# Kernel tuning notes

Hardware: AMD Instinct MI355X
Metric: run time of the kernel (lower is better)

The kernel has to match this reference:

```python
import jax, jax.numpy as jnp
import numpy as np

N, IN_DIM, HID, K, TOP_M = 131072, 512, 128, 256, 32


def setup_inputs() -> dict:
    key = jax.random.key(0)
    ks = jax.random.split(key, 16)
    s_in = 1.0 / np.sqrt(IN_DIM)
    s_h = 1.0 / np.sqrt(HID)
    return {
        "h0": jax.random.normal(ks[0], (N, IN_DIM), jnp.float32),
        "W1": jax.random.uniform(ks[1], (IN_DIM, HID), jnp.float32, -s_in, s_in),
        "b1": jax.random.uniform(ks[2], (HID,), jnp.float32, -s_in, s_in),
        "W2": jax.random.uniform(ks[3], (HID, HID), jnp.float32, -s_h, s_h),
        "b2": jax.random.uniform(ks[4], (HID,), jnp.float32, -s_h, s_h),
        "Wm": jax.random.uniform(ks[5], (HID, HID), jnp.float32, -s_h, s_h),
        "bm": jax.random.uniform(ks[6], (HID,), jnp.float32, -s_h, s_h),
        "Wt": jax.random.uniform(ks[7], (HID, HID), jnp.float32, -s_h, s_h),
        "bt": jax.random.uniform(ks[8], (HID,), jnp.float32, -s_h, s_h),
        "Wp": jax.random.uniform(ks[9], (HID, HID), jnp.float32, -s_h, s_h),
        "bp": jax.random.uniform(ks[10], (HID,), jnp.float32, -s_h, s_h),
        "cb_m": jax.random.normal(ks[11], (K, HID), jnp.float32),
        "cb_t": jax.random.normal(ks[12], (K, HID), jnp.float32),
        "cb_p": jax.random.normal(ks[13], (K, HID), jnp.float32),
        "ws": jax.random.uniform(ks[14], (HID,), jnp.float32, -s_h, s_h),
        "wb": jax.random.uniform(ks[15], (1,), jnp.float32, -s_h, s_h),
    }


def _l2n(x):
    return x / jnp.clip(jnp.linalg.norm(x, axis=-1, keepdims=True), 1e-12, None)


def _cos_dist(z, cb):
    # cosine-sim VQ codebook 'distance': [N, K] similarity matrix
    return jnp.einsum("nd,kd->nk", _l2n(z), _l2n(cb))


def reference(h0, W1, b1, W2, b2, Wm, bm, Wt, bt, Wp, bp, cb_m, cb_t, cb_p, ws, wb):
    # encoder MLP
    H = jax.nn.relu(jax.nn.relu(h0 @ W1 + b1) @ W2 + b2)  # [N, HID]
    dist_m = _cos_dist(H @ Wm + bm, cb_m)  # [N, K]
    dist_t = _cos_dist(H @ Wt + bt, cb_t)
    dist_p = _cos_dist(H @ Wp + bp, cb_p)
    # default path: argmin over codebook axis
    k_m = jnp.argmin(dist_m, axis=-1)
    k_t = jnp.argmin(dist_t, axis=-1)
    k_p = jnp.argmin(dist_p, axis=-1)
    codes = jnp.stack([k_m, k_t, k_p], axis=-1)  # [N, 3]
    alpha = jax.nn.sigmoid(H @ ws + wb[0])  # [N]
    n = codes.shape[0]
    M = min(TOP_M, n)
    _, key_idx = jax.lax.top_k(alpha, M)
    key_idx = jnp.clip(key_idx, 0, n - 1)
    return codes, key_idx, codes[key_idx]
```

## Files before the change

kernel.cpp:

```cpp
#include <hip/hip_runtime.h>

#define NROWS   131072
#define INDIM   512
#define HIDD    128
#define KCB     256

#define OFF_A     0u
#define OFF_CV    98304u
#define OFF_LOG   99072u
#define OFF_HIST  230144u
#define OFF_META  295680u
#define OFF_LISTA 295696u
#define OFF_LISTB 295824u
#define LISTB_CAP 2048u

__device__ __forceinline__ unsigned order_key(float f) {
    unsigned u = __float_as_uint(f);
    return u ^ ((u & 0x80000000u) ? 0xFFFFFFFFu : 0x80000000u);
}

__global__ __launch_bounds__(256) void vq_precompute(
    const float* __restrict__ Wm, const float* __restrict__ bm,
    const float* __restrict__ Wt, const float* __restrict__ bt,
    const float* __restrict__ Wp, const float* __restrict__ bp,
    const float* __restrict__ cbm, const float* __restrict__ cbt, const float* __restrict__ cbp,
    float* __restrict__ A, float* __restrict__ cv)
{
    const int c  = blockIdx.x >> 3;
    const int jg = (blockIdx.x & 7) * 16;
    const float* W  = (c == 0) ? Wm  : (c == 1) ? Wt  : Wp;
    const float* bb = (c == 0) ? bm  : (c == 1) ? bt  : bp;
    const float* cb = (c == 0) ? cbm : (c == 1) ? cbt : cbp;
    const int k = threadIdx.x;
    const float4* cbr = (const float4*)(cb + (size_t)k * HIDD);
    float s = 0.f;
    for (int d = 0; d < HIDD / 4; ++d) {
        float4 x = cbr[d];
        s += x.x * x.x + x.y * x.y + x.z * x.z + x.w * x.w;
    }
    const float rn = 1.f / fmaxf(sqrtf(s), 1e-12f);
    for (int j = jg; j < jg + 16; ++j) {
        const float4* wr = (const float4*)(W + (size_t)j * HIDD);
        float acc = 0.f;
        for (int d = 0; d < HIDD / 4; ++d) {
            float4 x = cbr[d]; float4 w = wr[d];
            acc += x.x * w.x + x.y * w.y + x.z * w.z + x.w * w.w;
        }
        A[((size_t)c * HIDD + j) * KCB + k] = acc * rn;
    }
    if (jg == 0) {
        const float4* br = (const float4*)bb;
        float acc = 0.f;
        for (int d = 0; d < HIDD / 4; ++d) {
            float4 x = cbr[d]; float4 w = br[d];
            acc += x.x * w.x + x.y * w.y + x.z * w.z + x.w * w.w;
        }
        cv[(size_t)c * KCB + k] = acc * rn;
    }
}

__global__ __launch_bounds__(256, 3) void vq_main(
    const float* __restrict__ h0, const float* __restrict__ W1, const float* __restrict__ b1,
    const float* __restrict__ W2, const float* __restrict__ b2,
    const float* __restrict__ A, const float* __restrict__ cv, const float* __restrict__ wsv,
    int* __restrict__ codes, float* __restrict__ logits, unsigned* __restrict__ hist)
{
    __shared__ float T[HIDD * 64];
    __shared__ float S[4096];

    const int t  = threadIdx.x;
    const int tx = t & 15;
    const int ty = t >> 4;
    const int row0 = blockIdx.x * 64;

    {
        float acc[4][8] = {};
        for (int kc = 0; kc < INDIM; kc += 16) {
            {
                const int rr = t >> 2, kq = (t & 3) * 4;
                float4 v = *(const float4*)(h0 + (size_t)(row0 + rr) * INDIM + kc + kq);
                S[(kq + 0) * 64 + rr] = v.x;
                S[(kq + 1) * 64 + rr] = v.y;
                S[(kq + 2) * 64 + rr] = v.z;
                S[(kq + 3) * 64 + rr] = v.w;
                const float4* src = (const float4*)(W1 + (size_t)kc * HIDD);
                float4* dst = (float4*)(S + 1024);
                dst[t]       = src[t];
                dst[t + 256] = src[t + 256];
            }
            __syncthreads();
            #pragma unroll 8
            for (int k = 0; k < 16; ++k) {
                float4 av  = *(const float4*)&S[k * 64 + 4 * ty];
                float4 b0  = *(const float4*)&S[1024 + k * HIDD + 4 * tx];
                float4 b1v = *(const float4*)&S[1024 + k * HIDD + 64 + 4 * tx];
                float aa[4] = {av.x, av.y, av.z, av.w};
                float bbv[8] = {b0.x, b0.y, b0.z, b0.w, b1v.x, b1v.y, b1v.z, b1v.w};
                #pragma unroll
                for (int r = 0; r < 4; ++r)
                    #pragma unroll
                    for (int j = 0; j < 8; ++j)
                        acc[r][j] = fmaf(aa[r], bbv[j], acc[r][j]);
            }
            __syncthreads();
        }
        float4 bv0 = *(const float4*)&b1[4 * tx];
        float4 bv1 = *(const float4*)&b1[4 * tx + 64];
        float ba[8] = {bv0.x, bv0.y, bv0.z, bv0.w, bv1.x, bv1.y, bv1.z, bv1.w};
        #pragma unroll
        for (int i = 0; i < 2; ++i)
            #pragma unroll
            for (int j = 0; j < 4; ++j) {
                const int c = 4 * tx + 64 * i + j;
                float4 col;
                col.x = fmaxf(acc[0][i * 4 + j] + ba[i * 4 + j], 0.f);
                col.y = fmaxf(acc[1][i * 4 + j] + ba[i * 4 + j], 0.f);
                col.z = fmaxf(acc[2][i * 4 + j] + ba[i * 4 + j], 0.f);
                col.w = fmaxf(acc[3][i * 4 + j] + ba[i * 4 + j], 0.f);
                *(float4*)&T[c * 64 + 4 * ty] = col;
            }
    }
    __syncthreads();

    {
        float acc[4][8] = {};
        for (int kc = 0; kc < HIDD; kc += 16) {
            const float4* src = (const float4*)(W2 + (size_t)kc * HIDD);
            float4* dst = (float4*)S;
            dst[t]       = src[t];
            dst[t + 256] = src[t + 256];
            __syncthreads();
            #pragma unroll 8
            for (int k = 0; k < 16; ++k) {
                float4 av  = *(const float4*)&T[(kc + k) * 64 + 4 * ty];
                float4 b0  = *(const float4*)&S[k * HIDD + 4 * tx];
                float4 b1v = *(const float4*)&S[k * HIDD + 64 + 4 * tx];
                float aa[4] = {av.x, av.y, av.z, av.w};
                float bbv[8] = {b0.x, b0.y, b0.z, b0.w, b1v.x, b1v.y, b1v.z, b1v.w};
                #pragma unroll
                for (int r = 0; r < 4; ++r)
                    #pragma unroll
                    for (int j = 0; j < 8; ++j)
                        acc[r][j] = fmaf(aa[r], bbv[j], acc[r][j]);
            }
            __syncthreads();
        }
        float4 bv0 = *(const float4*)&b2[4 * tx];
        float4 bv1 = *(const float4*)&b2[4 * tx + 64];
        float ba[8] = {bv0.x, bv0.y, bv0.z, bv0.w, bv1.x, bv1.y, bv1.z, bv1.w};
        #pragma unroll
        for (int i = 0; i < 2; ++i)
            #pragma unroll
            for (int j = 0; j < 4; ++j) {
                const int c = 4 * tx + 64 * i + j;
                float4 col;
                col.x = fmaxf(acc[0][i * 4 + j] + ba[i * 4 + j], 0.f);
                col.y = fmaxf(acc[1][i * 4 + j] + ba[i * 4 + j], 0.f);
                col.z = fmaxf(acc[2][i * 4 + j] + ba[i * 4 + j], 0.f);
                col.w = fmaxf(acc[3][i * 4 + j] + ba[i * 4 + j], 0.f);
                *(float4*)&T[c * 64 + 4 * ty] = col;
            }
    }
    __syncthreads();

    for (int cbk = 0; cbk < 3; ++cbk) {
        float acc[4][16] = {};
        for (int kc = 0; kc < HIDD; kc += 16) {
            const float4* src = (const float4*)(A + ((size_t)(cbk * HIDD + kc)) * KCB);
            float4* dst = (float4*)S;
            #pragma unroll
            for (int i = 0; i < 4; ++i) dst[t + 256 * i] = src[t + 256 * i];
            __syncthreads();
            #pragma unroll 4
            for (int k = 0; k < 16; ++k) {
                float4 av = *(const float4*)&T[(kc + k) * 64 + 4 * ty];
                float aa[4] = {av.x, av.y, av.z, av.w};
                #pragma unroll
                for (int i = 0; i < 4; ++i) {
                    float4 bv = *(const float4*)&S[k * KCB + 4 * tx + 64 * i];
                    float bbv[4] = {bv.x, bv.y, bv.z, bv.w};
                    #pragma unroll
                    for (int r = 0; r < 4; ++r)
                        #pragma unroll
                        for (int j = 0; j < 4; ++j)
                            acc[r][i * 4 + j] = fmaf(aa[r], bbv[j], acc[r][i * 4 + j]);
                }
            }
            __syncthreads();
        }
        float mv[4] = {3.4e38f, 3.4e38f, 3.4e38f, 3.4e38f};
        int   mi[4] = {0, 0, 0, 0};
        #pragma unroll
        for (int i = 0; i < 4; ++i) {
            float4 cvv = *(const float4*)&cv[cbk * KCB + 4 * tx + 64 * i];
            float ca[4] = {cvv.x, cvv.y, cvv.z, cvv.w};
            #pragma unroll
            for (int j = 0; j < 4; ++j) {
                const int c = 64 * i + 4 * tx + j;
                #pragma unroll
                for (int r = 0; r < 4; ++r) {
                    float v = acc[r][i * 4 + j] + ca[j];
                    if (v < mv[r]) { mv[r] = v; mi[r] = c; }
                }
            }
        }
        #pragma unroll
        for (int d = 1; d < 16; d <<= 1) {
            #pragma unroll
            for (int r = 0; r < 4; ++r) {
                float ov = __shfl_xor(mv[r], d);
                int   oi = __shfl_xor(mi[r], d);
                if (ov < mv[r] || (ov == mv[r] && oi < mi[r])) { mv[r] = ov; mi[r] = oi; }
            }
        }
        if (tx == 0) {
            #pragma unroll
            for (int r = 0; r < 4; ++r)
                codes[(size_t)(row0 + 4 * ty + r) * 3 + cbk] = mi[r];
        }
    }

    if (t < HIDD) S[t] = wsv[t];
    __syncthreads();
    if (t < 64) {
        float s = 0.f;
        #pragma unroll 8
        for (int k = 0; k < HIDD; ++k) s = fmaf(T[k * 64 + t], S[k], s);
        logits[row0 + t] = s;
        atomicAdd(&hist[order_key(s) >> 16], 1u);
    }
}

__global__ __launch_bounds__(1024) void vq_findp(const unsigned* __restrict__ hist,
                                                 unsigned* __restrict__ meta)
{
    __shared__ unsigned Tb[1024];
    __shared__ unsigned sIg, sPg;
    const int t = threadIdx.x;
    unsigned s = 0;
    const uint4* hv = (const uint4*)(hist + (size_t)t * 64);
    for (int j = 0; j < 16; ++j) { uint4 h = hv[j]; s += h.x + h.y + h.z + h.w; }
    Tb[t] = s;
    __syncthreads();
    for (int d = 1; d < 1024; d <<= 1) {
        unsigned v = (t + d < 1024) ? Tb[t + d] : 0u;
        __syncthreads();
        Tb[t] += v;
        __syncthreads();
    }
    const unsigned Ti = Tb[t];
    const unsigned P  = Ti - s;
    if (P < 32u && Ti >= 32u) { sIg = (unsigned)t; sPg = P; }
    __syncthreads();
    const int ig = (int)sIg;
    const unsigned Pg = sPg;
    if (t < 64) {
        unsigned c = hist[ig * 64 + t];
        unsigned Tw = c;
        #pragma unroll
        for (int d = 1; d < 64; d <<= 1) {
            unsigned v = __shfl_down(Tw, d);
            if (t + d < 64) Tw += v;
        }
        unsigned Pl = Pg + Tw - c;
        if (Pl < 32u && Pl + c >= 32u) { meta[2] = (unsigned)(ig * 64 + t); meta[3] = Pl; }
    }
}

__global__ __launch_bounds__(256) void vq_collect(
    const float* __restrict__ logits, unsigned* __restrict__ meta,
    unsigned* __restrict__ listA, unsigned* __restrict__ listB)
{
    const int i = blockIdx.x * 256 + threadIdx.x;
    const unsigned key = order_key(logits[i]);
    const unsigned p = meta[2];
    const unsigned b = key >> 16;
    if (b > p) {
        unsigned idx = atomicAdd(&meta[0], 1u);
        if (idx < 64u) { listA[2 * idx] = key; listA[2 * idx + 1] = (unsigned)i; }
    } else if (b == p) {
        unsigned idx = atomicAdd(&meta[1], 1u);
        if (idx < LISTB_CAP) { listB[2 * idx] = key; listB[2 * idx + 1] = (unsigned)i; }
    }
}

__global__ void vq_final(const unsigned* __restrict__ meta,
                         const unsigned* __restrict__ listA, const unsigned* __restrict__ listB,
                         const int* __restrict__ codes,
                         int* __restrict__ outki, int* __restrict__ outsel)
{
    if (threadIdx.x != 0 || blockIdx.x != 0) return;
    unsigned nAv = meta[0]; int nA = (nAv > 64u) ? 64 : (int)nAv;
    unsigned nBv = meta[1]; int nB = (nBv > LISTB_CAP) ? (int)LISTB_CAP : (int)nBv;
    unsigned lk = 0u, li = 0u;
    bool first = true;
    for (int m = 0; m < 32; ++m) {
        int best = -1; unsigned bk = 0u, bi = 0u;
        for (int j = 0; j < nA + nB; ++j) {
            unsigned k2, ix;
            if (j < nA) { k2 = listA[2 * j]; ix = listA[2 * j + 1]; }
            else        { int jj = j - nA; k2 = listB[2 * jj]; ix = listB[2 * jj + 1]; }
            if (!first) {
                bool after = (k2 < lk) || (k2 == lk && ix > li);
                if (!after) continue;
            }
            if (best < 0 || k2 > bk || (k2 == bk && ix < bi)) { best = j; bk = k2; bi = ix; }
        }
        if (best < 0) { bk = lk; bi = 0u; }
        outki[m] = (int)bi;
        lk = bk; li = bi; first = false;
    }
    for (int m = 0; m < 32; ++m) {
        const int idx = outki[m];
        outsel[3 * m + 0] = codes[3 * idx + 0];
        outsel[3 * m + 1] = codes[3 * idx + 1];
        outsel[3 * m + 2] = codes[3 * idx + 2];
    }
}

extern "C" void kernel_launch(void* const* d_in, const int* in_sizes, int n_in,
                              void* d_out, int out_size, void* d_ws, size_t ws_size,
                              hipStream_t stream)
{
    (void)in_sizes; (void)n_in; (void)out_size; (void)ws_size;

    const float* h0  = (const float*)d_in[0];
    const float* W1  = (const float*)d_in[1];
    const float* b1  = (const float*)d_in[2];
    const float* W2  = (const float*)d_in[3];
    const float* b2  = (const float*)d_in[4];
    const float* Wm  = (const float*)d_in[5];
    const float* bm  = (const float*)d_in[6];
    const float* Wt  = (const float*)d_in[7];
    const float* bt  = (const float*)d_in[8];
    const float* Wp  = (const float*)d_in[9];
    const float* bp  = (const float*)d_in[10];
    const float* cbm = (const float*)d_in[11];
    const float* cbt = (const float*)d_in[12];
    const float* cbp = (const float*)d_in[13];
    const float* wsv = (const float*)d_in[14];

    float*    wsf   = (float*)d_ws;
    unsigned* wsu   = (unsigned*)d_ws;
    float*    A     = wsf + OFF_A;
    float*    cvv   = wsf + OFF_CV;
    float*    logit = wsf + OFF_LOG;
    unsigned* hist  = wsu + OFF_HIST;
    unsigned* meta  = wsu + OFF_META;
    unsigned* listA = wsu + OFF_LISTA;
    unsigned* listB = wsu + OFF_LISTB;

    int* codes  = (int*)d_out;
    int* outki  = codes + (size_t)NROWS * 3;
    int* outsel = outki + 32;

    hipMemsetAsync((void*)hist, 0, (65536 + 16) * sizeof(unsigned), stream);
    vq_precompute<<<24, 256, 0, stream>>>(Wm, bm, Wt, bt, Wp, bp, cbm, cbt, cbp, A, cvv);
    vq_main<<<NROWS / 64, 256, 0, stream>>>(h0, W1, b1, W2, b2, A, cvv, wsv, codes, logit, hist);
    vq_findp<<<1, 1024, 0, stream>>>(hist, meta);
    vq_collect<<<NROWS / 256, 256, 0, stream>>>(logit, meta, listA, listB);
    vq_final<<<1, 64, 0, stream>>>(meta, listA, listB, codes, outki, outsel);
}
```

Measured before the change: 882.1 us.

## Double rows per block, prefetch tiles to registers, parallelize final top-k

Raises the rows per block from 64 to 128, so each thread computes an 8x8 (or 8x16) register tile and reuses every shared-memory weight load across twice as many rows. Global loads for the next tile are now issued into registers before the barrier, and the end-of-loop barriers are dropped, which hides some load latency and cuts synchronisation. The histogram memset is folded into the precompute kernel to save a launch. The single-thread serial top-32 selection is replaced by a 256-thread rank-counting selection. In exchange, register pressure and LDS use per block roughly double, which lowers occupancy (launch bounds relaxed from 3 to 2 blocks per CU) and halves the number of blocks.

```diff
diff --git a/kernel.cpp b/kernel.cpp
--- a/kernel.cpp
+++ b/kernel.cpp
@@ -4,6 +4,7 @@
 #define INDIM   512
 #define HIDD    128
 #define KCB     256
+#define RPB     128
 
 #define OFF_A     0u
 #define OFF_CV    98304u
@@ -24,8 +25,11 @@
     const float* __restrict__ Wt, const float* __restrict__ bt,
     const float* __restrict__ Wp, const float* __restrict__ bp,
     const float* __restrict__ cbm, const float* __restrict__ cbt, const float* __restrict__ cbp,
-    float* __restrict__ A, float* __restrict__ cv)
-{
+    float* __restrict__ A, float* __restrict__ cv, unsigned* __restrict__ hist)
+{
+    for (unsigned i = blockIdx.x * 256u + threadIdx.x; i < 65536u + 16u; i += 24u * 256u)
+        hist[i] = 0u;
+
     const int c  = blockIdx.x >> 3;
     const int jg = (blockIdx.x & 7) * 16;
     const float* W  = (c == 0) ? Wm  : (c == 1) ? Wt  : Wp;
@@ -59,137 +63,164 @@
     }
 }
 
-__global__ __launch_bounds__(256, 3) void vq_main(
-    const float* __restrict__ h0, const float* __restrict__ W1, const float* __restrict__ b1,
-    const float* __restrict__ W2, const float* __restrict__ b2,
-    const float* __restrict__ A, const float* __restrict__ cv, const float* __restrict__ wsv,
+__global__ __launch_bounds__(256, 2) void vq_main(
+    const float* __restrict__ h0, const float* __restrict__ W1, const float* __restrict__ bias1,
+    const float* __restrict__ W2, const float* __restrict__ bias2,
+    const float* __restrict__ Amat, const float* __restrict__ cv, const float* __restrict__ wsv,
     int* __restrict__ codes, float* __restrict__ logits, unsigned* __restrict__ hist)
 {
-    __shared__ float T[HIDD * 64];
+    __shared__ float T[HIDD * RPB];
     __shared__ float S[4096];
 
     const int t  = threadIdx.x;
     const int tx = t & 15;
     const int ty = t >> 4;
-    const int row0 = blockIdx.x * 64;
+    const int row0 = blockIdx.x * RPB;
 
     {
-        float acc[4][8] = {};
+        float acc[8][8] = {};
+        const int srow = t >> 1;
+        const int sq   = (t & 1) * 8;
+        const float* hp = h0 + (size_t)(row0 + srow) * INDIM + sq;
         for (int kc = 0; kc < INDIM; kc += 16) {
-            {
-                const int rr = t >> 2, kq = (t & 3) * 4;
-                float4 v = *(const float4*)(h0 + (size_t)(row0 + rr) * INDIM + kc + kq);
-                S[(kq + 0) * 64 + rr] = v.x;
-                S[(kq + 1) * 64 + rr] = v.y;
-                S[(kq + 2) * 64 + rr] = v.z;
-                S[(kq + 3) * 64 + rr] = v.w;
-                const float4* src = (const float4*)(W1 + (size_t)kc * HIDD);
-                float4* dst = (float4*)(S + 1024);
-                dst[t]       = src[t];
-                dst[t + 256] = src[t + 256];
-            }
-            __syncthreads();
-            #pragma unroll 8
+            float4 ha = *(const float4*)(hp + kc);
+            float4 hb = *(const float4*)(hp + kc + 4);
+            const float4* wsrc = (const float4*)(W1 + (size_t)kc * HIDD);
+            float4 w0 = wsrc[t];
+            float4 w1 = wsrc[t + 256];
+            __syncthreads();
+            S[(sq + 0) * RPB + srow] = ha.x;
+            S[(sq + 1) * RPB + srow] = ha.y;
+            S[(sq + 2) * RPB + srow] = ha.z;
+            S[(sq + 3) * RPB + srow] = ha.w;
+            S[(sq + 4) * RPB + srow] = hb.x;
+            S[(sq + 5) * RPB + srow] = hb.y;
+            S[(sq + 6) * RPB + srow] = hb.z;
+            S[(sq + 7) * RPB + srow] = hb.w;
+            float4* wdst = (float4*)(S + 2048);
+            wdst[t]       = w0;
+            wdst[t + 256] = w1;
+            __syncthreads();
+            #pragma unroll
             for (int k = 0; k < 16; ++k) {
-                float4 av  = *(const float4*)&S[k * 64 + 4 * ty];
-                float4 b0  = *(const float4*)&S[1024 + k * HIDD + 4 * tx];
-                float4 b1v = *(const float4*)&S[1024 + k * HIDD + 64 + 4 * tx];
-                float aa[4] = {av.x, av.y, av.z, av.w};
-                float bbv[8] = {b0.x, b0.y, b0.z, b0.w, b1v.x, b1v.y, b1v.z, b1v.w};
+                float4 a0 = *(const float4*)&S[k * RPB + 8 * ty];
+                float4 a1 = *(const float4*)&S[k * RPB + 8 * ty + 4];
+                float4 b0 = *(const float4*)&S[2048 + k * HIDD + 4 * tx];
+                float4 b1v = *(const float4*)&S[2048 + k * HIDD + 4 * tx + 64];
+                float aa[8] = {a0.x, a0.y, a0.z, a0.w, a1.x, a1.y, a1.z, a1.w};
+                float bb[8] = {b0.x, b0.y, b0.z, b0.w, b1v.x, b1v.y, b1v.z, b1v.w};
                 #pragma unroll
-                for (int r = 0; r < 4; ++r)
+                for (int r = 0; r < 8; ++r)
                     #pragma unroll
                     for (int j = 0; j < 8; ++j)
-                        acc[r][j] = fmaf(aa[r], bbv[j], acc[r][j]);
-            }
-            __syncthreads();
-        }
-        float4 bv0 = *(const float4*)&b1[4 * tx];
-        float4 bv1 = *(const float4*)&b1[4 * tx + 64];
+                        acc[r][j] = fmaf(aa[r], bb[j], acc[r][j]);
+            }
+        }
+        float4 bv0 = *(const float4*)&bias1[4 * tx];
+        float4 bv1 = *(const float4*)&bias1[4 * tx + 64];
         float ba[8] = {bv0.x, bv0.y, bv0.z, bv0.w, bv1.x, bv1.y, bv1.z, bv1.w};
         #pragma unroll
         for (int i = 0; i < 2; ++i)
             #pragma unroll
             for (int j = 0; j < 4; ++j) {
                 const int c = 4 * tx + 64 * i + j;
-                float4 col;
-                col.x = fmaxf(acc[0][i * 4 + j] + ba[i * 4 + j], 0.f);
-                col.y = fmaxf(acc[1][i * 4 + j] + ba[i * 4 + j], 0.f);
-                col.z = fmaxf(acc[2][i * 4 + j] + ba[i * 4 + j], 0.f);
-                col.w = fmaxf(acc[3][i * 4 + j] + ba[i * 4 + j], 0.f);
-                *(float4*)&T[c * 64 + 4 * ty] = col;
-            }
-    }
-    __syncthreads();
+                float4 lo, hi;
+                lo.x = fmaxf(acc[0][i * 4 + j] + ba[i * 4 + j], 0.f);
+                lo.y = fmaxf(acc[1][i * 4 + j] + ba[i * 4 + j], 0.f);
+                lo.z = fmaxf(acc[2][i * 4 + j] + ba[i * 4 + j], 0.f);
+                lo.w = fmaxf(acc[3][i * 4 + j] + ba[i * 4 + j], 0.f);
+                hi.x = fmaxf(acc[4][i * 4 + j] + ba[i * 4 + j], 0.f);
+                hi.y = fmaxf(acc[5][i * 4 + j] + ba[i * 4 + j], 0.f);
+                hi.z = fmaxf(acc[6][i * 4 + j] + ba[i * 4 + j], 0.f);
+                hi.w = fmaxf(acc[7][i * 4 + j] + ba[i * 4 + j], 0.f);
+                *(float4*)&T[c * RPB + 8 * ty]     = lo;
+                *(float4*)&T[c * RPB + 8 * ty + 4] = hi;
+            }
+    }
 
     {
-        float acc[4][8] = {};
+        float acc[8][8] = {};
         for (int kc = 0; kc < HIDD; kc += 16) {
-            const float4* src = (const float4*)(W2 + (size_t)kc * HIDD);
-            float4* dst = (float4*)S;
-            dst[t]       = src[t];
-            dst[t + 256] = src[t + 256];
-            __syncthreads();
-            #pragma unroll 8
+            const float4* wsrc = (const float4*)(W2 + (size_t)kc * HIDD);
+            float4 w0 = wsrc[t];
+            float4 w1 = wsrc[t + 256];
+            __syncthreads();
+            float4* wdst = (float4*)S;
+            wdst[t]       = w0;
+            wdst[t + 256] = w1;
+            __syncthreads();
+            #pragma unroll
             for (int k = 0; k < 16; ++k) {
-                float4 av  = *(const float4*)&T[(kc + k) * 64 + 4 * ty];
-                float4 b0  = *(const float4*)&S[k * HIDD + 4 * tx];
-                float4 b1v = *(const float4*)&S[k * HIDD + 64 + 4 * tx];
-                float aa[4] = {av.x, av.y, av.z, av.w};
-                float bbv[8] = {b0.x, b0.y, b0.z, b0.w, b1v.x, b1v.y, b1v.z, b1v.w};
+                float4 a0 = *(const float4*)&T[(kc + k) * RPB + 8 * ty];
+                float4 a1 = *(const float4*)&T[(kc + k) * RPB + 8 * ty + 4];
+                float4 b0 = *(const float4*)&S[k * HIDD + 4 * tx];
+                float4 b1v = *(const float4*)&S[k * HIDD + 4 * tx + 64];
+                float aa[8] = {a0.x, a0.y, a0.z, a0.w, a1.x, a1.y, a1.z, a1.w};
+                float bb[8] = {b0.x, b0.y, b0.z, b0.w, b1v.x, b1v.y, b1v.z, b1v.w};
                 #pragma unroll
-                for (int r = 0; r < 4; ++r)
+                for (int r = 0; r < 8; ++r)
                     #pragma unroll
                     for (int j = 0; j < 8; ++j)
-                        acc[r][j] = fmaf(aa[r], bbv[j], acc[r][j]);
-            }
-            __syncthreads();
-        }
-        float4 bv0 = *(const float4*)&b2[4 * tx];
-        float4 bv1 = *(const float4*)&b2[4 * tx + 64];
+                        acc[r][j] = fmaf(aa[r], bb[j], acc[r][j]);
+            }
+        }
+        __syncthreads();
+        float4 bv0 = *(const float4*)&bias2[4 * tx];
+        float4 bv1 = *(const float4*)&bias2[4 * tx + 64];
         float ba[8] = {bv0.x, bv0.y, bv0.z, bv0.w, bv1.x, bv1.y, bv1.z, bv1.w};
         #pragma unroll
         for (int i = 0; i < 2; ++i)
             #pragma unroll
             for (int j = 0; j < 4; ++j) {
                 const int c = 4 * tx + 64 * i + j;
-                float4 col;
-                col.x = fmaxf(acc[0][i * 4 + j] + ba[i * 4 + j], 0.f);
-                col.y = fmaxf(acc[1][i * 4 + j] + ba[i * 4 + j], 0.f);
-                col.z = fmaxf(acc[2][i * 4 + j] + ba[i * 4 + j], 0.f);
-                col.w = fmaxf(acc[3][i * 4 + j] + ba[i * 4 + j], 0.f);
-                *(float4*)&T[c * 64 + 4 * ty] = col;
-            }
-    }
-    __syncthreads();
+                float4 lo, hi;
+                lo.x = fmaxf(acc[0][i * 4 + j] + ba[i * 4 + j], 0.f);
+                lo.y = fmaxf(acc[1][i * 4 + j] + ba[i * 4 + j], 0.f);
+                lo.z = fmaxf(acc[2][i * 4 + j] + ba[i * 4 + j], 0.f);
+                lo.w = fmaxf(acc[3][i * 4 + j] + ba[i * 4 + j], 0.f);
+                hi.x = fmaxf(acc[4][i * 4 + j] + ba[i * 4 + j], 0.f);
+                hi.y = fmaxf(acc[5][i * 4 + j] + ba[i * 4 + j], 0.f);
+                hi.z = fmaxf(acc[6][i * 4 + j] + ba[i * 4 + j], 0.f);
+                hi.w = fmaxf(acc[7][i * 4 + j] + ba[i * 4 + j], 0.f);
+                *(float4*)&T[c * RPB + 8 * ty]     = lo;
+                *(float4*)&T[c * RPB + 8 * ty + 4] = hi;
+            }
+    }
 
     for (int cbk = 0; cbk < 3; ++cbk) {
-        float acc[4][16] = {};
+        float acc[8][16] = {};
         for (int kc = 0; kc < HIDD; kc += 16) {
-            const float4* src = (const float4*)(A + ((size_t)(cbk * HIDD + kc)) * KCB);
+            const float4* src = (const float4*)(Amat + ((size_t)cbk * HIDD + kc) * KCB);
+            float4 s0 = src[t];
+            float4 s1 = src[t + 256];
+            float4 s2 = src[t + 512];
+            float4 s3 = src[t + 768];
+            __syncthreads();
             float4* dst = (float4*)S;
-            #pragma unroll
-            for (int i = 0; i < 4; ++i) dst[t + 256 * i] = src[t + 256 * i];
-            __syncthreads();
-            #pragma unroll 4
+            dst[t]       = s0;
+            dst[t + 256] = s1;
+            dst[t + 512] = s2;
+            dst[t + 768] = s3;
+            __syncthreads();
+            #pragma unroll
             for (int k = 0; k < 16; ++k) {
-                float4 av = *(const float4*)&T[(kc + k) * 64 + 4 * ty];
-                float aa[4] = {av.x, av.y, av.z, av.w};
+                float4 a0 = *(const float4*)&T[(kc + k) * RPB + 8 * ty];
+                float4 a1 = *(const float4*)&T[(kc + k) * RPB + 8 * ty + 4];
+                float aa[8] = {a0.x, a0.y, a0.z, a0.w, a1.x, a1.y, a1.z, a1.w};
                 #pragma unroll
                 for (int i = 0; i < 4; ++i) {
                     float4 bv = *(const float4*)&S[k * KCB + 4 * tx + 64 * i];
-                    float bbv[4] = {bv.x, bv.y, bv.z, bv.w};
+                    float bb[4] = {bv.x, bv.y, bv.z, bv.w};
                     #pragma unroll
-                    for (int r = 0; r < 4; ++r)
+                    for (int r = 0; r < 8; ++r)
                         #pragma unroll
                         for (int j = 0; j < 4; ++j)
-                            acc[r][i * 4 + j] = fmaf(aa[r], bbv[j], acc[r][i * 4 + j]);
+                            acc[r][i * 4 + j] = fmaf(aa[r], bb[j], acc[r][i * 4 + j]);
                 }
             }
-            __syncthreads();
-        }
-        float mv[4] = {3.4e38f, 3.4e38f, 3.4e38f, 3.4e38f};
-        int   mi[4] = {0, 0, 0, 0};
+        }
+        float mv[8] = {3.4e38f, 3.4e38f, 3.4e38f, 3.4e38f, 3.4e38f, 3.4e38f, 3.4e38f, 3.4e38f};
+        int   mi[8] = {0, 0, 0, 0, 0, 0, 0, 0};
         #pragma unroll
         for (int i = 0; i < 4; ++i) {
             float4 cvv = *(const float4*)&cv[cbk * KCB + 4 * tx + 64 * i];
@@ -198,7 +229,7 @@
             for (int j = 0; j < 4; ++j) {
                 const int c = 64 * i + 4 * tx + j;
                 #pragma unroll
-                for (int r = 0; r < 4; ++r) {
+                for (int r = 0; r < 8; ++r) {
                     float v = acc[r][i * 4 + j] + ca[j];
                     if (v < mv[r]) { mv[r] = v; mi[r] = c; }
                 }
@@ -207,7 +238,7 @@
         #pragma unroll
         for (int d = 1; d < 16; d <<= 1) {
             #pragma unroll
-            for (int r = 0; r < 4; ++r) {
+            for (int r = 0; r < 8; ++r) {
                 float ov = __shfl_xor(mv[r], d);
                 int   oi = __shfl_xor(mi[r], d);
                 if (ov < mv[r] || (ov == mv[r] && oi < mi[r])) { mv[r] = ov; mi[r] = oi; }
@@ -215,17 +246,18 @@
         }
         if (tx == 0) {
             #pragma unroll
-            for (int r = 0; r < 4; ++r)
-                codes[(size_t)(row0 + 4 * ty + r) * 3 + cbk] = mi[r];
-        }
-    }
-
+            for (int r = 0; r < 8; ++r)
+                codes[(size_t)(row0 + 8 * ty + r) * 3 + cbk] = mi[r];
+        }
+    }
+
+    __syncthreads();
     if (t < HIDD) S[t] = wsv[t];
     __syncthreads();
-    if (t < 64) {
+    if (t < RPB) {
         float s = 0.f;
         #pragma unroll 8
-        for (int k = 0; k < HIDD; ++k) s = fmaf(T[k * 64 + t], S[k], s);
+        for (int k = 0; k < HIDD; ++k) s = fmaf(T[k * RPB + t], S[k], s);
         logits[row0 + t] = s;
         atomicAdd(&hist[order_key(s) >> 16], 1u);
     }
@@ -284,38 +316,38 @@
     }
 }
 
-__global__ void vq_final(const unsigned* __restrict__ meta,
-                         const unsigned* __restrict__ listA, const unsigned* __restrict__ listB,
-                         const int* __restrict__ codes,
-                         int* __restrict__ outki, int* __restrict__ outsel)
-{
-    if (threadIdx.x != 0 || blockIdx.x != 0) return;
-    unsigned nAv = meta[0]; int nA = (nAv > 64u) ? 64 : (int)nAv;
-    unsigned nBv = meta[1]; int nB = (nBv > LISTB_CAP) ? (int)LISTB_CAP : (int)nBv;
-    unsigned lk = 0u, li = 0u;
-    bool first = true;
-    for (int m = 0; m < 32; ++m) {
-        int best = -1; unsigned bk = 0u, bi = 0u;
-        for (int j = 0; j < nA + nB; ++j) {
-            unsigned k2, ix;
-            if (j < nA) { k2 = listA[2 * j]; ix = listA[2 * j + 1]; }
-            else        { int jj = j - nA; k2 = listB[2 * jj]; ix = listB[2 * jj + 1]; }
-            if (!first) {
-                bool after = (k2 < lk) || (k2 == lk && ix > li);
-                if (!after) continue;
-            }
-            if (best < 0 || k2 > bk || (k2 == bk && ix < bi)) { best = j; bk = k2; bi = ix; }
-        }
-        if (best < 0) { bk = lk; bi = 0u; }
-        outki[m] = (int)bi;
-        lk = bk; li = bi; first = false;
-    }
-    for (int m = 0; m < 32; ++m) {
-        const int idx = outki[m];
-        outsel[3 * m + 0] = codes[3 * idx + 0];
-        outsel[3 * m + 1] = codes[3 * idx + 1];
-        outsel[3 * m + 2] = codes[3 * idx + 2];
-    }
+__global__ __launch_bounds__(256) void vq_final(
+    const unsigned* __restrict__ meta,
+    const unsigned* __restrict__ listA, const unsigned* __restrict__ listB,
+    const int* __restrict__ codes,
+    int* __restrict__ outki, int* __restrict__ outsel)
+{
+    __shared__ unsigned Ks[64 + LISTB_CAP];
+    __shared__ unsigned Is[64 + LISTB_CAP];
+    __shared__ int sel[32];
+    const int t = threadIdx.x;
+    const unsigned nAv = meta[0];
+    const unsigned nBv = meta[1];
+    const int nA = (nAv > 64u) ? 64 : (int)nAv;
+    const int nB = (nBv > LISTB_CAP) ? (int)LISTB_CAP : (int)nBv;
+    const int n  = nA + nB;
+    for (int j = t; j < n; j += 256) {
+        if (j < nA) { Ks[j] = listA[2 * j]; Is[j] = listA[2 * j + 1]; }
+        else        { int jj = j - nA; Ks[j] = listB[2 * jj]; Is[j] = listB[2 * jj + 1]; }
+    }
+    __syncthreads();
+    for (int j = t; j < n; j += 256) {
+        const unsigned kj = Ks[j], ij = Is[j];
+        int rank = 0;
+        for (int m = 0; m < n; ++m) {
+            const unsigned km = Ks[m], im = Is[m];
+            rank += (km > kj) || (km == kj && im < ij);
+        }
+        if (rank < 32) sel[rank] = (int)ij;
+    }
+    __syncthreads();
+    if (t < 32) outki[t] = sel[t];
+    if (t < 96) outsel[t] = codes[3 * sel[t / 3] + (t % 3)];
 }
 
 extern "C" void kernel_launch(void* const* d_in, const int* in_sizes, int n_in,
@@ -354,10 +386,9 @@
     int* outki  = codes + (size_t)NROWS * 3;
     int* outsel = outki + 32;
 
-    hipMemsetAsync((void*)hist, 0, (65536 + 16) * sizeof(unsigned), stream);
-    vq_precompute<<<24, 256, 0, stream>>>(Wm, bm, Wt, bt, Wp, bp, cbm, cbt, cbp, A, cvv);
-    vq_main<<<NROWS / 64, 256, 0, stream>>>(h0, W1, b1, W2, b2, A, cvv, wsv, codes, logit, hist);
+    vq_precompute<<<24, 256, 0, stream>>>(Wm, bm, Wt, bt, Wp, bp, cbm, cbt, cbp, A, cvv, hist);
+    vq_main<<<NROWS / RPB, 256, 0, stream>>>(h0, W1, b1, W2, b2, A, cvv, wsv, codes, logit, hist);
     vq_findp<<<1, 1024, 0, stream>>>(hist, meta);
     vq_collect<<<NROWS / 256, 256, 0, stream>>>(logit, meta, listA, listB);
-    vq_final<<<1, 64, 0, stream>>>(meta, listA, listB, codes, outki, outsel);
-}
+    vq_final<<<1, 256, 0, stream>>>(meta, listA, listB, codes, outki, outsel);
+}
```

Result: faster. 714.6 us (-19.0%).
